# Kernel optimization log

Measured on AMD Instinct MI355X. Metric: run time of the kernel, lower is better.

## Reference

```python
import jax, jax.numpy as jnp
import numpy as np

EPS = 1.0    # Lennard-Jones well depth
SIGMA = 1.0  # Lennard-Jones length scale


def setup_inputs() -> dict:
    key = jax.random.key(0)
    k1, k2, k3, k4 = jax.random.split(key, 4)
    B, N, D = 2, 4096, 3
    q = jax.random.normal(k1, (B, N, D), dtype=jnp.float32)
    p = jax.random.normal(k2, (B, N, D), dtype=jnp.float32)
    # masses strictly positive, away from zero
    m = jax.random.uniform(k3, (B, N, 1), dtype=jnp.float32, minval=0.5, maxval=1.5)
    t = jax.random.uniform(k4, (), dtype=jnp.float32)
    return {"q": q, "p": p, "m": m, "t": t}


def _lj_pair_force(q):
    # disp[b,i,j,:] = q[b,i,:] - q[b,j,:]   (torch: unsqueeze(-2) - unsqueeze(-3))
    disp = q[..., :, None, :] - q[..., None, :, :]          # [B,N,N,3]
    r2 = jnp.sum(disp * disp, axis=-1)                      # [B,N,N]
    mask = r2 > 0.0                                          # excludes i==j diagonal
    safe_r2 = jnp.where(mask, r2, 1.0)
    inv_r2 = jnp.where(mask, 1.0 / safe_r2, 0.0)
    s2 = (SIGMA * SIGMA) * inv_r2
    s6 = s2 * s2 * s2
    # LJ force on i from j: 24*eps*(2*s12 - s6)/r^2 * disp
    coeff = 24.0 * EPS * inv_r2 * s6 * (2.0 * s6 - 1.0)      # [B,N,N]
    force = coeff[..., None] * disp                          # [B,N,N,3]
    # sum(axis=-2): sum over partner index j
    return jnp.sum(force, axis=-2)                           # [B,N,3]


def reference(q, p, m, t):
    dq = p / m                   # Experiment.dq
    dp = _lj_pair_force(q)       # BasePairPotential.dp with LJ force
    return (dq, dp)
```

## Files before the change

kernel.cpp:

```cpp
#include <hip/hip_runtime.h>

#define BATCH    2
#define NPART    4096
#define NTHREADS 512
#define IBLK     16
#define ILANES   8
#define JCH      (NTHREADS / ILANES)
#define JLEN     (NPART / JCH)
#define NIB      (NPART / IBLK)

typedef float v2f __attribute__((ext_vector_type(2)));

__global__ __launch_bounds__(NTHREADS, 4) void lj_fused(
        const float* __restrict__ q, const float* __restrict__ p,
        const float* __restrict__ m, float* __restrict__ dq,
        float* __restrict__ dp) {
    __shared__ float red[JCH * 6 * ILANES];

    const int ib = blockIdx.x;
    const int b  = blockIdx.y;
    const int t  = threadIdx.x;
    const int il = t & (ILANES - 1);
    const int jc = t >> 3;

    const float* qb = q + (size_t)b * NPART * 3;

    const int i0 = ib * IBLK + il;
    const int i1 = i0 + ILANES;
    const v2f qx = {qb[i0 * 3 + 0], qb[i1 * 3 + 0]};
    const v2f qy = {qb[i0 * 3 + 1], qb[i1 * 3 + 1]};
    const v2f qz = {qb[i0 * 3 + 2], qb[i1 * 3 + 2]};

    v2f fx = (v2f)0.0f, fy = (v2f)0.0f, fz = (v2f)0.0f;

    const float4* jq4 = (const float4*)(qb + (size_t)jc * JLEN * 3);

    #pragma unroll 2
    for (int it = 0; it < JLEN / 4; ++it) {
        const float4 A = jq4[3 * it + 0];
        const float4 B = jq4[3 * it + 1];
        const float4 C = jq4[3 * it + 2];
        const float jxs[4] = {A.x, A.w, B.z, C.y};
        const float jys[4] = {A.y, B.x, B.w, C.z};
        const float jzs[4] = {A.z, B.y, C.x, C.w};
        #pragma unroll
        for (int u = 0; u < 4; ++u) {
            const v2f dx = qx - (v2f)jxs[u];
            const v2f dy = qy - (v2f)jys[u];
            const v2f dz = qz - (v2f)jzs[u];
            v2f r2 = dx * dx;
            r2 = __builtin_elementwise_fma(dy, dy, r2);
            r2 = __builtin_elementwise_fma(dz, dz, r2);
            v2f inv;
            inv.x = (r2.x > 0.0f) ? __builtin_amdgcn_rcpf(r2.x) : 0.0f;
            inv.y = (r2.y > 0.0f) ? __builtin_amdgcn_rcpf(r2.y) : 0.0f;
            const v2f inv2 = inv * inv;
            const v2f s6 = inv2 * inv;
            const v2f c1 = __builtin_elementwise_fma((v2f)48.0f, s6, (v2f)(-24.0f));
            const v2f coeff = (inv * s6) * c1;
            fx = __builtin_elementwise_fma(coeff, dx, fx);
            fy = __builtin_elementwise_fma(coeff, dy, fy);
            fz = __builtin_elementwise_fma(coeff, dz, fz);
        }
    }

    red[(jc * 6 + 0) * ILANES + il] = fx.x;
    red[(jc * 6 + 1) * ILANES + il] = fx.y;
    red[(jc * 6 + 2) * ILANES + il] = fy.x;
    red[(jc * 6 + 3) * ILANES + il] = fy.y;
    red[(jc * 6 + 4) * ILANES + il] = fz.x;
    red[(jc * 6 + 5) * ILANES + il] = fz.y;
    __syncthreads();

    if (t < 48) {
        const int c   = t >> 4;
        const int ii  = t & 15;
        const int h   = ii >> 3;
        const int il2 = ii & 7;
        const int slot = c * 2 + h;
        float s = 0.0f;
        #pragma unroll
        for (int k = 0; k < JCH; ++k) {
            s += red[(k * 6 + slot) * ILANES + il2];
        }
        const size_t gi = (size_t)b * NPART + ib * IBLK + ii;
        dp[gi * 3 + c] = s;
        dq[gi * 3 + c] = p[gi * 3 + c] / m[gi];
    }
}

extern "C" void kernel_launch(void* const* d_in, const int* in_sizes, int n_in,
                              void* d_out, int out_size, void* d_ws, size_t ws_size,
                              hipStream_t stream) {
    const float* q = (const float*)d_in[0];
    const float* p = (const float*)d_in[1];
    const float* m = (const float*)d_in[2];

    const int n_elem = BATCH * NPART * 3;
    float* dq_out = (float*)d_out;
    float* dp_out = (float*)d_out + n_elem;

    dim3 grid(NIB, BATCH);
    lj_fused<<<grid, NTHREADS, 0, stream>>>(q, p, m, dq_out, dp_out);
}
```

Measured before the change: 19.09 us.

## Shrink i-tile, skip diagonal masking off-diagonal, reduce forces via wave shuffles

Reworks the blocking: 256 threads with 4 i-particles per block (2 lanes × 2 packed), giving 1024×2 blocks and longer j-chunks per thread. The r2>0 mask is kept only in the wave that covers the diagonal j-chunk, and all other waves run an unmasked rcp loop. The shared-memory reduction over all j-chunks becomes xor-shuffle reductions within each wave followed by a small cross-wave sum. The intent is to cut per-pair compare/select work and reduction overhead and to raise block count. In exchange each block reloads far more j data per i-particle, and duplicate positions off the diagonal would now give infinities.

```diff
diff --git a/kernel.cpp b/kernel.cpp
--- a/kernel.cpp
+++ b/kernel.cpp
@@ -2,26 +2,70 @@
 
 #define BATCH    2
 #define NPART    4096
-#define NTHREADS 512
-#define IBLK     16
-#define ILANES   8
+#define NTHREADS 256
+#define IBLK     4
+#define ILANES   2
 #define JCH      (NTHREADS / ILANES)
 #define JLEN     (NPART / JCH)
 #define NIB      (NPART / IBLK)
+#define NWAVES   (NTHREADS / 64)
 
 typedef float v2f __attribute__((ext_vector_type(2)));
 
-__global__ __launch_bounds__(NTHREADS, 4) void lj_fused(
+template <bool MASKED>
+__device__ inline void lj_body(float jx, float jy, float jz,
+                               v2f qx, v2f qy, v2f qz,
+                               v2f& fx, v2f& fy, v2f& fz) {
+    const v2f dx = qx - (v2f)jx;
+    const v2f dy = qy - (v2f)jy;
+    const v2f dz = qz - (v2f)jz;
+    v2f r2 = dx * dx;
+    r2 = __builtin_elementwise_fma(dy, dy, r2);
+    r2 = __builtin_elementwise_fma(dz, dz, r2);
+    v2f inv;
+    if (MASKED) {
+        inv.x = (r2.x > 0.0f) ? __builtin_amdgcn_rcpf(r2.x) : 0.0f;
+        inv.y = (r2.y > 0.0f) ? __builtin_amdgcn_rcpf(r2.y) : 0.0f;
+    } else {
+        inv.x = __builtin_amdgcn_rcpf(r2.x);
+        inv.y = __builtin_amdgcn_rcpf(r2.y);
+    }
+    const v2f inv2 = inv * inv;
+    const v2f s6 = inv2 * inv;
+    const v2f c1 = __builtin_elementwise_fma((v2f)48.0f, s6, (v2f)(-24.0f));
+    const v2f coeff = (inv * s6) * c1;
+    fx = __builtin_elementwise_fma(coeff, dx, fx);
+    fy = __builtin_elementwise_fma(coeff, dy, fy);
+    fz = __builtin_elementwise_fma(coeff, dz, fz);
+}
+
+template <bool MASKED>
+__device__ inline void chunk_loop(const float4* __restrict__ jq4,
+                                  v2f qx, v2f qy, v2f qz,
+                                  v2f& fx, v2f& fy, v2f& fz) {
+    #pragma unroll 2
+    for (int it = 0; it < JLEN / 4; ++it) {
+        const float4 A = jq4[3 * it + 0];
+        const float4 B = jq4[3 * it + 1];
+        const float4 C = jq4[3 * it + 2];
+        lj_body<MASKED>(A.x, A.y, A.z, qx, qy, qz, fx, fy, fz);
+        lj_body<MASKED>(A.w, B.x, B.y, qx, qy, qz, fx, fy, fz);
+        lj_body<MASKED>(B.z, B.w, C.x, qx, qy, qz, fx, fy, fz);
+        lj_body<MASKED>(C.y, C.z, C.w, qx, qy, qz, fx, fy, fz);
+    }
+}
+
+__global__ __launch_bounds__(NTHREADS, 8) void lj_fused(
         const float* __restrict__ q, const float* __restrict__ p,
         const float* __restrict__ m, float* __restrict__ dq,
         float* __restrict__ dp) {
-    __shared__ float red[JCH * 6 * ILANES];
+    __shared__ float red2[NWAVES * 12];
 
     const int ib = blockIdx.x;
     const int b  = blockIdx.y;
     const int t  = threadIdx.x;
-    const int il = t & (ILANES - 1);
-    const int jc = t >> 3;
+    const int il = t & 1;
+    const int jc = t >> 1;
 
     const float* qb = q + (size_t)b * NPART * 3;
 
@@ -35,54 +79,38 @@
 
     const float4* jq4 = (const float4*)(qb + (size_t)jc * JLEN * 3);
 
-    #pragma unroll 2
-    for (int it = 0; it < JLEN / 4; ++it) {
-        const float4 A = jq4[3 * it + 0];
-        const float4 B = jq4[3 * it + 1];
-        const float4 C = jq4[3 * it + 2];
-        const float jxs[4] = {A.x, A.w, B.z, C.y};
-        const float jys[4] = {A.y, B.x, B.w, C.z};
-        const float jzs[4] = {A.z, B.y, C.x, C.w};
-        #pragma unroll
-        for (int u = 0; u < 4; ++u) {
-            const v2f dx = qx - (v2f)jxs[u];
-            const v2f dy = qy - (v2f)jys[u];
-            const v2f dz = qz - (v2f)jzs[u];
-            v2f r2 = dx * dx;
-            r2 = __builtin_elementwise_fma(dy, dy, r2);
-            r2 = __builtin_elementwise_fma(dz, dz, r2);
-            v2f inv;
-            inv.x = (r2.x > 0.0f) ? __builtin_amdgcn_rcpf(r2.x) : 0.0f;
-            inv.y = (r2.y > 0.0f) ? __builtin_amdgcn_rcpf(r2.y) : 0.0f;
-            const v2f inv2 = inv * inv;
-            const v2f s6 = inv2 * inv;
-            const v2f c1 = __builtin_elementwise_fma((v2f)48.0f, s6, (v2f)(-24.0f));
-            const v2f coeff = (inv * s6) * c1;
-            fx = __builtin_elementwise_fma(coeff, dx, fx);
-            fy = __builtin_elementwise_fma(coeff, dy, fy);
-            fz = __builtin_elementwise_fma(coeff, dz, fz);
-        }
+    const int diagc = ib >> 3;
+    if (__any(jc == diagc)) {
+        chunk_loop<true >(jq4, qx, qy, qz, fx, fy, fz);
+    } else {
+        chunk_loop<false>(jq4, qx, qy, qz, fx, fy, fz);
     }
 
-    red[(jc * 6 + 0) * ILANES + il] = fx.x;
-    red[(jc * 6 + 1) * ILANES + il] = fx.y;
-    red[(jc * 6 + 2) * ILANES + il] = fy.x;
-    red[(jc * 6 + 3) * ILANES + il] = fy.y;
-    red[(jc * 6 + 4) * ILANES + il] = fz.x;
-    red[(jc * 6 + 5) * ILANES + il] = fz.y;
+    #pragma unroll
+    for (int msk = 2; msk <= 32; msk <<= 1) {
+        fx.x += __shfl_xor(fx.x, msk); fx.y += __shfl_xor(fx.y, msk);
+        fy.x += __shfl_xor(fy.x, msk); fy.y += __shfl_xor(fy.y, msk);
+        fz.x += __shfl_xor(fz.x, msk); fz.y += __shfl_xor(fz.y, msk);
+    }
+    const int w    = t >> 6;
+    const int lane = t & 63;
+    if (lane < 2) {
+        float* r = &red2[w * 12 + lane * 6];
+        r[0] = fx.x; r[1] = fx.y;
+        r[2] = fy.x; r[3] = fy.y;
+        r[4] = fz.x; r[5] = fz.y;
+    }
     __syncthreads();
 
-    if (t < 48) {
-        const int c   = t >> 4;
-        const int ii  = t & 15;
-        const int h   = ii >> 3;
-        const int il2 = ii & 7;
-        const int slot = c * 2 + h;
+    if (t < 12) {
+        const int c   = t >> 2;
+        const int ii  = t & 3;
+        const int h   = ii >> 1;
+        const int il2 = ii & 1;
+        const int slot = il2 * 6 + c * 2 + h;
         float s = 0.0f;
         #pragma unroll
-        for (int k = 0; k < JCH; ++k) {
-            s += red[(k * 6 + slot) * ILANES + il2];
-        }
+        for (int wv = 0; wv < NWAVES; ++wv) s += red2[wv * 12 + slot];
         const size_t gi = (size_t)b * NPART + ib * IBLK + ii;
         dp[gi * 3 + c] = s;
         dq[gi * 3 + c] = p[gi * 3 + c] / m[gi];
```

Result: slower. 21.11 us (+10.6%).

## Split j-range across blocks with atomic accumulation and skip masking off-diagonal tiles

Applied to the files above, without the earlier changes.

Restructures the work decomposition. Each block now covers a 128-particle i-tile and one of 16 j-segments, with each wave walking its own slice of j using wave-uniform (scalar) loads of j positions. Partial forces are reduced in shared memory and then atomically added into dp, which is zeroed by a memset beforehand. The r2>0 mask is applied only to tiles that contain the diagonal. This adds a memset launch and atomic traffic in exchange for fewer threads per i particle, cheaper j loads and less masking work.

```diff
diff --git a/kernel.cpp b/kernel.cpp
--- a/kernel.cpp
+++ b/kernel.cpp
@@ -3,89 +3,101 @@
 #define BATCH    2
 #define NPART    4096
 #define NTHREADS 512
-#define IBLK     16
-#define ILANES   8
-#define JCH      (NTHREADS / ILANES)
-#define JLEN     (NPART / JCH)
-#define NIB      (NPART / IBLK)
+#define NWAVES   8
+#define ITILE    128
+#define NIT      (NPART / ITILE)
+#define NJS      16
+#define JSEG     (NPART / NJS)
+#define JPW      (JSEG / NWAVES)
 
 typedef float v2f __attribute__((ext_vector_type(2)));
 
-__global__ __launch_bounds__(NTHREADS, 4) void lj_fused(
+template <bool MASKED>
+__device__ inline void lj_j(float jx, float jy, float jz,
+                            v2f qx, v2f qy, v2f qz,
+                            v2f& fx, v2f& fy, v2f& fz) {
+    const v2f dx = qx - (v2f)jx;
+    const v2f dy = qy - (v2f)jy;
+    const v2f dz = qz - (v2f)jz;
+    v2f r2 = dx * dx;
+    r2 = __builtin_elementwise_fma(dy, dy, r2);
+    r2 = __builtin_elementwise_fma(dz, dz, r2);
+    v2f inv;
+    if (MASKED) {
+        inv.x = (r2.x > 0.0f) ? __builtin_amdgcn_rcpf(r2.x) : 0.0f;
+        inv.y = (r2.y > 0.0f) ? __builtin_amdgcn_rcpf(r2.y) : 0.0f;
+    } else {
+        inv.x = __builtin_amdgcn_rcpf(r2.x);
+        inv.y = __builtin_amdgcn_rcpf(r2.y);
+    }
+    const v2f inv2 = inv * inv;
+    const v2f s6 = inv2 * inv;
+    const v2f c1 = __builtin_elementwise_fma((v2f)48.0f, s6, (v2f)(-24.0f));
+    const v2f coeff = (inv * s6) * c1;
+    fx = __builtin_elementwise_fma(coeff, dx, fx);
+    fy = __builtin_elementwise_fma(coeff, dy, fy);
+    fz = __builtin_elementwise_fma(coeff, dz, fz);
+}
+
+__global__ __launch_bounds__(NTHREADS, 8) void lj_fused(
         const float* __restrict__ q, const float* __restrict__ p,
         const float* __restrict__ m, float* __restrict__ dq,
         float* __restrict__ dp) {
-    __shared__ float red[JCH * 6 * ILANES];
+    __shared__ float red[NWAVES][64][7];
 
-    const int ib = blockIdx.x;
-    const int b  = blockIdx.y;
+    const int it = blockIdx.x;
+    const int js = blockIdx.y;
+    const int b  = blockIdx.z;
     const int t  = threadIdx.x;
-    const int il = t & (ILANES - 1);
-    const int jc = t >> 3;
+    const int l  = t & 63;
+    const int w  = t >> 6;
 
     const float* qb = q + (size_t)b * NPART * 3;
 
-    const int i0 = ib * IBLK + il;
-    const int i1 = i0 + ILANES;
-    const v2f qx = {qb[i0 * 3 + 0], qb[i1 * 3 + 0]};
-    const v2f qy = {qb[i0 * 3 + 1], qb[i1 * 3 + 1]};
-    const v2f qz = {qb[i0 * 3 + 2], qb[i1 * 3 + 2]};
+    const int i0 = it * ITILE + 2 * l;
+    const float2* qi2 = (const float2*)(qb + (size_t)i0 * 3);
+    const float2 a0 = qi2[0];
+    const float2 a1 = qi2[1];
+    const float2 a2 = qi2[2];
+    const v2f qx = {a0.x, a1.y};
+    const v2f qy = {a0.y, a2.x};
+    const v2f qz = {a1.x, a2.y};
 
     v2f fx = (v2f)0.0f, fy = (v2f)0.0f, fz = (v2f)0.0f;
 
-    const float4* jq4 = (const float4*)(qb + (size_t)jc * JLEN * 3);
+    const int wv = __builtin_amdgcn_readfirstlane(w);
+    const float* jq = qb + (size_t)(js * JSEG + wv * JPW) * 3;
 
-    #pragma unroll 2
-    for (int it = 0; it < JLEN / 4; ++it) {
-        const float4 A = jq4[3 * it + 0];
-        const float4 B = jq4[3 * it + 1];
-        const float4 C = jq4[3 * it + 2];
-        const float jxs[4] = {A.x, A.w, B.z, C.y};
-        const float jys[4] = {A.y, B.x, B.w, C.z};
-        const float jzs[4] = {A.z, B.y, C.x, C.w};
-        #pragma unroll
-        for (int u = 0; u < 4; ++u) {
-            const v2f dx = qx - (v2f)jxs[u];
-            const v2f dy = qy - (v2f)jys[u];
-            const v2f dz = qz - (v2f)jzs[u];
-            v2f r2 = dx * dx;
-            r2 = __builtin_elementwise_fma(dy, dy, r2);
-            r2 = __builtin_elementwise_fma(dz, dz, r2);
-            v2f inv;
-            inv.x = (r2.x > 0.0f) ? __builtin_amdgcn_rcpf(r2.x) : 0.0f;
-            inv.y = (r2.y > 0.0f) ? __builtin_amdgcn_rcpf(r2.y) : 0.0f;
-            const v2f inv2 = inv * inv;
-            const v2f s6 = inv2 * inv;
-            const v2f c1 = __builtin_elementwise_fma((v2f)48.0f, s6, (v2f)(-24.0f));
-            const v2f coeff = (inv * s6) * c1;
-            fx = __builtin_elementwise_fma(coeff, dx, fx);
-            fy = __builtin_elementwise_fma(coeff, dy, fy);
-            fz = __builtin_elementwise_fma(coeff, dz, fz);
-        }
+    if (js == (it >> 1)) {
+        #pragma unroll 8
+        for (int k = 0; k < JPW; ++k)
+            lj_j<true >(jq[3 * k], jq[3 * k + 1], jq[3 * k + 2],
+                        qx, qy, qz, fx, fy, fz);
+    } else {
+        #pragma unroll 8
+        for (int k = 0; k < JPW; ++k)
+            lj_j<false>(jq[3 * k], jq[3 * k + 1], jq[3 * k + 2],
+                        qx, qy, qz, fx, fy, fz);
     }
 
-    red[(jc * 6 + 0) * ILANES + il] = fx.x;
-    red[(jc * 6 + 1) * ILANES + il] = fx.y;
-    red[(jc * 6 + 2) * ILANES + il] = fy.x;
-    red[(jc * 6 + 3) * ILANES + il] = fy.y;
-    red[(jc * 6 + 4) * ILANES + il] = fz.x;
-    red[(jc * 6 + 5) * ILANES + il] = fz.y;
+    red[w][l][0] = fx.x;  red[w][l][1] = fx.y;
+    red[w][l][2] = fy.x;  red[w][l][3] = fy.y;
+    red[w][l][4] = fz.x;  red[w][l][5] = fz.y;
     __syncthreads();
 
-    if (t < 48) {
-        const int c   = t >> 4;
-        const int ii  = t & 15;
-        const int h   = ii >> 3;
-        const int il2 = ii & 7;
-        const int slot = c * 2 + h;
+    if (t < 384) {
+        const int il = t / 3;
+        const int c  = t - 3 * il;
+        const int lx = il >> 1;
+        const int hx = il & 1;
         float s = 0.0f;
         #pragma unroll
-        for (int k = 0; k < JCH; ++k) {
-            s += red[(k * 6 + slot) * ILANES + il2];
+        for (int ww = 0; ww < NWAVES; ++ww) s += red[ww][lx][c * 2 + hx];
+        const size_t go = (size_t)b * (NPART * 3) + (size_t)it * (ITILE * 3) + t;
+        atomicAdd(&dp[go], s);
+        if (js == 0) {
+            dq[go] = p[go] / m[go / 3];
         }
-        const size_t gi = (size_t)b * NPART + ib * IBLK + ii;
-        dp[gi * 3 + c] = s;
-        dq[gi * 3 + c] = p[gi * 3 + c] / m[gi];
     }
 }
 
@@ -100,6 +112,8 @@
     float* dq_out = (float*)d_out;
     float* dp_out = (float*)d_out + n_elem;
 
-    dim3 grid(NIB, BATCH);
+    hipMemsetAsync(dp_out, 0, (size_t)n_elem * sizeof(float), stream);
+
+    dim3 grid(NIT, NJS, BATCH);
     lj_fused<<<grid, NTHREADS, 0, stream>>>(q, p, m, dq_out, dp_out);
 }
```

Result: slower. 21.72 us (+13.8%).
